# Kernel tuning notes

Measured on AMD Instinct MI355X. Metric: run time of the kernel, lower is better.

Reference implementation:

```python
import jax, jax.numpy as jnp
import numpy as np
import math

H = 16          # n_head
N_EMBD = 1024
EPS = 1e-5      # torch LayerNorm default


def setup_inputs() -> dict:
    key = jax.random.key(0)
    ks = jax.random.split(key, 6)
    B, T, C = 2, 2048, 1024
    x = jax.random.normal(ks[0], (B, T, C), dtype=jnp.float32)
    s = 0.02  # GPT-2 style init scale keeps softmax logits sane
    Wq = jax.random.normal(ks[1], (C, N_EMBD), dtype=jnp.float32) * s
    Wk = jax.random.normal(ks[2], (C, N_EMBD), dtype=jnp.float32) * s
    Wv = jax.random.normal(ks[3], (C, N_EMBD), dtype=jnp.float32) * s
    Wo = jax.random.normal(ks[4], (N_EMBD, C), dtype=jnp.float32) * s
    return {
        "x": x,
        "Wq": Wq, "bq": jnp.zeros((N_EMBD,), jnp.float32),
        "Wk": Wk, "bk": jnp.zeros((N_EMBD,), jnp.float32),
        "Wv": Wv, "bv": jnp.zeros((N_EMBD,), jnp.float32),
        "Wo": Wo, "bo": jnp.zeros((C,), jnp.float32),
        "gamma": jnp.ones((C,), jnp.float32),
        "beta": jnp.zeros((C,), jnp.float32),
    }


def reference(x, Wq, bq, Wk, bk, Wv, bv, Wo, bo, gamma, beta):
    B, T, _ = x.shape
    Dh = N_EMBD // H
    # projections -> (B, H, T, Dh)
    def split_heads(y):
        return y.reshape(B, T, H, Dh).transpose(0, 2, 1, 3)
    q = split_heads(x @ Wq + bq)
    k = split_heads(x @ Wk + bk)
    v = split_heads(x @ Wv + bv)
    # naive causal attention: explicit (B,H,T,T) scores
    att = jnp.einsum("bhtd,bhsd->bhts", q, k) * (1.0 / math.sqrt(Dh))
    causal = jnp.tril(jnp.ones((T, T), dtype=bool))
    att = jnp.where(causal[None, None], att, -jnp.inf)
    att = jax.nn.softmax(att, axis=-1)
    o = jnp.einsum("bhts,bhsd->bhtd", att, v)
    o = o.transpose(0, 2, 1, 3).reshape(B, T, N_EMBD)
    y = o @ Wo + bo
    # LayerNorm (dropout is identity at p=0 / eval)
    mu = jnp.mean(y, axis=-1, keepdims=True)
    var = jnp.var(y, axis=-1, keepdims=True)
    return (y - mu) * jax.lax.rsqrt(var + EPS) * gamma + beta
```

## Files before the change

kernel.cpp:

```cpp
#include <hip/hip_runtime.h>
#include <stdint.h>
#include <stddef.h>

typedef __attribute__((ext_vector_type(8))) short short8;
typedef __attribute__((ext_vector_type(4))) float f32x4;
typedef __attribute__((ext_vector_type(16))) float f32x16;
typedef __attribute__((ext_vector_type(4))) unsigned short us4;
typedef __attribute__((ext_vector_type(4))) unsigned u32x4;

#define DEVI static __device__ __forceinline__

DEVI unsigned short f2bf(float f) {
  unsigned u = __builtin_bit_cast(unsigned, f);
  u += 0x7FFFu + ((u >> 16) & 1u);
  return (unsigned short)(u >> 16);
}

DEVI float bf2f(unsigned short u) {
  return __builtin_bit_cast(float, ((unsigned)u) << 16);
}

DEVI f32x4 mfma16(short8 a, short8 b, f32x4 c) {
  return __builtin_amdgcn_mfma_f32_16x16x32_bf16(a, b, c, 0, 0, 0);
}

DEVI f32x16 mfma32(short8 a, short8 b, f32x16 c) {
  return __builtin_amdgcn_mfma_f32_32x32x16_bf16(a, b, c, 0, 0, 0);
}

DEVI unsigned cvtpk(float lo, float hi) {
  unsigned r;
  asm("v_cvt_pk_bf16_f32 %0, %1, %2" : "=v"(r) : "v"(lo), "v"(hi));
  return r;
}

DEVI void plswap(unsigned& a, unsigned& b) {
  asm("v_permlane32_swap_b32 %0, %1" : "+v"(a), "+v"(b));
}

DEVI float ex2(float x) {
  float r;
  asm("v_exp_f32 %0, %1" : "=v"(r) : "v"(x));
  return r;
}

DEVI float mx3(float a, float b, float c) {
  float r;
  asm("v_max3_f32 %0, %1, %2, %3" : "=v"(r) : "v"(a), "v"(b), "v"(c));
  return r;
}

DEVI f32x16 zero16() {
  f32x16 z;
#pragma unroll
  for (int i = 0; i < 16; ++i) z[i] = 0.f;
  return z;
}

DEVI void glds16(const void* g, void* l) {
  __builtin_amdgcn_global_load_lds(
      (const __attribute__((address_space(1))) void*)g,
      (__attribute__((address_space(3))) void*)l, 16, 0, 0);
}

__global__ __launch_bounds__(256) void k_cvt_x(const float* __restrict__ x,
                                               unsigned short* __restrict__ xb) {
  size_t i = ((size_t)blockIdx.x * 256 + threadIdx.x) * 8;
  f32x4 a = *(const f32x4*)(x + i);
  f32x4 b = *(const f32x4*)(x + i + 4);
  short8 v;
#pragma unroll
  for (int j = 0; j < 4; ++j) {
    v[j] = (short)f2bf(a[j]);
    v[4 + j] = (short)f2bf(b[j]);
  }
  *(short8*)(xb + i) = v;
}

__global__ __launch_bounds__(256) void k_twT4(const float* __restrict__ W0,
                                              const float* __restrict__ W1,
                                              const float* __restrict__ W2,
                                              const float* __restrict__ W3,
                                              unsigned short* __restrict__ WT) {
  __shared__ float tile[64][65];
  const int z = blockIdx.z;
  const float* W = (z == 0) ? W0 : (z == 1) ? W1 : (z == 2) ? W2 : W3;
  unsigned short* out = WT + (size_t)z * 1024 * 1024;
  const int n0 = blockIdx.x * 64, k0 = blockIdx.y * 64;
  const int t = threadIdx.x, rr = t >> 4, cc = (t & 15) * 4;
#pragma unroll
  for (int i = 0; i < 4; ++i) {
    int row = i * 16 + rr;
    f32x4 v = *(const f32x4*)(W + (size_t)(k0 + row) * 1024 + n0 + cc);
#pragma unroll
    for (int j = 0; j < 4; ++j) tile[row][cc + j] = v[j];
  }
  __syncthreads();
#pragma unroll
  for (int i = 0; i < 4; ++i) {
    int nrow = i * 16 + rr;
    us4 u;
#pragma unroll
    for (int j = 0; j < 4; ++j) u[j] = f2bf(tile[cc + j][nrow]);
    *(us4*)(out + (size_t)(n0 + nrow) * 1024 + k0 + cc) = u;
  }
}

template <bool SWAP>
DEVI void gemm_core2(const unsigned short* __restrict__ A,
                     const unsigned short* __restrict__ Bt,
                     int mt, int nt, char* lds, f32x4 (&acc)[4][4]) {
  const int t = threadIdx.x;
  const int l = t & 63, c = l & 15, g = l >> 4;
  const int w = t >> 6, wr = w >> 1, wc = w & 1;
  const int srow = t >> 3;
  const int sxor = (((t & 7) ^ (srow & 7))) * 8;
  const unsigned short* Ab = A + (size_t)(mt * 128 + srow) * 1024 + sxor;
  const unsigned short* Bb = Bt + (size_t)(nt * 128 + srow) * 1024 + sxor;
  const int key = (c & 7);

  auto STAGE = [&](int kt, int buf) {
    char* lb = lds + buf * 32768;
#pragma unroll
    for (int i = 0; i < 4; ++i) {
      glds16(Ab + (size_t)i * 32 * 1024 + kt * 64, lb + i * 4096 + t * 16);
      glds16(Bb + (size_t)i * 32 * 1024 + kt * 64, lb + 16384 + i * 4096 + t * 16);
    }
  };

  STAGE(0, 0);
  asm volatile("s_waitcnt vmcnt(0)" ::: "memory");
  __builtin_amdgcn_s_barrier();
  asm volatile("" ::: "memory");
  for (int kt = 0; kt < 16; ++kt) {
    const int cur = kt & 1;
    if (kt < 15) STAGE(kt + 1, cur ^ 1);
    const char* lb = lds + cur * 32768;
#pragma unroll
    for (int ks = 0; ks < 2; ++ks) {
      short8 af[4], bfr[4];
#pragma unroll
      for (int m = 0; m < 4; ++m)
        af[m] = *(const short8*)(lb + (wr * 64 + m * 16 + c) * 128 +
                                 ((ks * 4 + g) ^ key) * 16);
#pragma unroll
      for (int n = 0; n < 4; ++n)
        bfr[n] = *(const short8*)(lb + 16384 + (wc * 64 + n * 16 + c) * 128 +
                                  ((ks * 4 + g) ^ key) * 16);
#pragma unroll
      for (int m = 0; m < 4; ++m)
#pragma unroll
        for (int n = 0; n < 4; ++n)
          acc[m][n] = SWAP ? mfma16(bfr[n], af[m], acc[m][n])
                           : mfma16(af[m], bfr[n], acc[m][n]);
    }
    asm volatile("s_waitcnt vmcnt(0)" ::: "memory");
    __builtin_amdgcn_s_barrier();
    asm volatile("" ::: "memory");
  }
}

template <bool SWAP>
DEVI void gemm_core3(const unsigned short* __restrict__ A,
                     const unsigned short* __restrict__ Bt,
                     int mt, int nt, char* lds, f32x4 (&acc)[8][4]) {
  const int t = threadIdx.x;
  const int l = t & 63, c = l & 15, g = l >> 4;
  const int w = t >> 6, wm = w >> 2, wn = w & 3;
  const int srow = t >> 3;
  const int sxor = ((t & 7) ^ (srow & 7)) * 8;
  const unsigned short* Ab = A + (size_t)(mt * 256 + srow) * 1024 + sxor;
  const unsigned short* Bb = Bt + (size_t)(nt * 256 + srow) * 1024 + sxor;
  const int key = c & 7;

  auto STAGE = [&](int kt, int buf) {
    char* lb = lds + buf * 65536;
#pragma unroll
    for (int i = 0; i < 4; ++i) {
      glds16(Ab + (size_t)(i * 64) * 1024 + kt * 64, lb + i * 8192 + t * 16);
      glds16(Bb + (size_t)(i * 64) * 1024 + kt * 64, lb + 32768 + i * 8192 + t * 16);
    }
  };

  STAGE(0, 0);
  asm volatile("s_waitcnt vmcnt(0)" ::: "memory");
  __builtin_amdgcn_s_barrier();
  asm volatile("" ::: "memory");
  for (int kt = 0; kt < 16; ++kt) {
    const int cur = kt & 1;
    if (kt < 15) STAGE(kt + 1, cur ^ 1);
    const char* la = lds + cur * 65536;
    const char* lbB = la + 32768;
    short8 bf[4][2];
#pragma unroll
    for (int fc = 0; fc < 4; ++fc)
#pragma unroll
      for (int ks = 0; ks < 2; ++ks) {
        int brow = wn * 64 + fc * 16 + c;
        bf[fc][ks] = *(const short8*)(lbB + brow * 128 + (((ks * 4 + g) ^ key) * 16));
      }
#pragma unroll
    for (int p = 0; p < 4; ++p) {
      short8 af[2][2];
#pragma unroll
      for (int r2 = 0; r2 < 2; ++r2)
#pragma unroll
        for (int ks = 0; ks < 2; ++ks) {
          int arow = wm * 128 + (2 * p + r2) * 16 + c;
          af[r2][ks] = *(const short8*)(la + arow * 128 + (((ks * 4 + g) ^ key) * 16));
        }
      __builtin_amdgcn_s_setprio(1);
#pragma unroll
      for (int ks = 0; ks < 2; ++ks)
#pragma unroll
        for (int r2 = 0; r2 < 2; ++r2)
#pragma unroll
          for (int fc = 0; fc < 4; ++fc)
            acc[2 * p + r2][fc] = SWAP ? mfma16(bf[fc][ks], af[r2][ks], acc[2 * p + r2][fc])
                                       : mfma16(af[r2][ks], bf[fc][ks], acc[2 * p + r2][fc]);
      __builtin_amdgcn_s_setprio(0);
    }
    asm volatile("s_waitcnt vmcnt(0)" ::: "memory");
    __builtin_amdgcn_s_barrier();
    asm volatile("" ::: "memory");
  }
}

__global__ __launch_bounds__(512) void k_gemm_qkv2(
    const unsigned short* __restrict__ A,
    const unsigned short* __restrict__ Wf,
    const float* __restrict__ b0, const float* __restrict__ b1, const float* __restrict__ b2,
    unsigned short* __restrict__ O0, unsigned short* __restrict__ O1,
    unsigned short* __restrict__ O2) {
  extern __shared__ char lds[];
  const int ntz = blockIdx.x, mt = blockIdx.y;
  const int z = ntz >> 2, ntl = ntz & 3;
  const float* bias = (z == 0) ? b0 : (z == 1) ? b1 : b2;
  unsigned short* out = (z == 0) ? O0 : (z == 1) ? O1 : O2;
  f32x4 acc[8][4];
#pragma unroll
  for (int m = 0; m < 8; ++m)
#pragma unroll
    for (int n = 0; n < 4; ++n) acc[m][n] = (f32x4){0.f, 0.f, 0.f, 0.f};
  const int t = threadIdx.x, l = t & 63, c = l & 15, g = l >> 4;
  const int w = t >> 6, wm = w >> 2, wn = w & 3;
  if (z < 2) {
    gemm_core3<true>(A, Wf, mt, ntz, lds, acc);
    const float sc = (z == 0) ? 0.18033688011f : 1.0f;
#pragma unroll
    for (int fc = 0; fc < 4; ++fc) {
      int colb = ntl * 256 + wn * 64 + fc * 16 + 4 * g;
      f32x4 bv4 = *(const f32x4*)(bias + colb);
      int h = colb >> 6, d = colb & 63;
#pragma unroll
      for (int fr = 0; fr < 8; ++fr) {
        int rowg = mt * 256 + wm * 128 + fr * 16 + c;
        int b = rowg >> 11, tt = rowg & 2047;
        us4 u;
#pragma unroll
        for (int r = 0; r < 4; ++r) u[r] = f2bf((acc[fr][fc][r] + bv4[r]) * sc);
        *(us4*)(out + ((size_t)(b * 16 + h) * 2048 + tt) * 64 + d) = u;
      }
    }
  } else {
    gemm_core3<false>(A, Wf, mt, ntz, lds, acc);
#pragma unroll
    for (int fc = 0; fc < 4; ++fc) {
      int colg = ntl * 256 + wn * 64 + fc * 16 + c;
      float bvv = bias[colg];
      int h = colg >> 6, d = colg & 63;
#pragma unroll
      for (int fr = 0; fr < 8; ++fr) {
        int rowg = mt * 256 + wm * 128 + fr * 16 + 4 * g;
        int b = rowg >> 11, tt = rowg & 2047;
        us4 u;
#pragma unroll
        for (int r = 0; r < 4; ++r) u[r] = f2bf(acc[fr][fc][r] + bvv);
        *(us4*)(out + ((size_t)(b * 16 + h) * 64 + d) * 2048 + tt) = u;
      }
    }
  }
}

__global__ __launch_bounds__(256) void k_gemm_proj(const unsigned short* __restrict__ A,
                                                   const unsigned short* __restrict__ Bt,
                                                   const float* __restrict__ bias,
                                                   float* __restrict__ Y) {
  __shared__ char lds[65536];
  f32x4 acc[4][4];
#pragma unroll
  for (int m = 0; m < 4; ++m)
#pragma unroll
    for (int n = 0; n < 4; ++n) acc[m][n] = (f32x4){0.f, 0.f, 0.f, 0.f};
  const int lin = blockIdx.y * 32 + blockIdx.x;
  const int nt = lin & 7, mt = lin >> 3;
  gemm_core2<true>(A, Bt, mt, nt, lds, acc);
  const int t = threadIdx.x, l = t & 63, c = l & 15, g = l >> 4;
  const int w = t >> 6, wr = w >> 1, wc = w & 1;
#pragma unroll
  for (int n = 0; n < 4; ++n) {
    int colb = nt * 128 + wc * 64 + n * 16 + 4 * g;
    f32x4 bv4 = *(const f32x4*)(bias + colb);
#pragma unroll
    for (int m = 0; m < 4; ++m) {
      int rowg = mt * 128 + wr * 64 + m * 16 + c;
      f32x4 o;
#pragma unroll
      for (int r = 0; r < 4; ++r) o[r] = acc[m][n][r] + bv4[r];
      *(f32x4*)(Y + (size_t)rowg * 1024 + colb) = o;
    }
  }
}

__global__ __launch_bounds__(128) void k_attn5(const unsigned short* __restrict__ Q,
                                               const unsigned short* __restrict__ K,
                                               const unsigned short* __restrict__ VT,
                                               unsigned short* __restrict__ O,
                                               unsigned short* __restrict__ P,
                                               float* __restrict__ ML) {
  __shared__ char lds[32768];
  const int bid = blockIdx.x;
  int qt, c0, nt, mode, bh;
  if (bid < 512) {
    mode = 1; qt = 16 + (bid >> 5); c0 = 0; nt = 16; bh = bid & 31;
  } else {
    int rem = bid - 512;
    int v = 16 - (rem >> 6);
    int sub = rem & 63;
    bh = sub & 31;
    if (sub < 32) { mode = 0; qt = v - 1;  c0 = 0;  nt = v; }
    else          { mode = 2; qt = v + 15; c0 = 16; nt = v; }
  }
  const int t = threadIdx.x;
  const int w = t >> 6, l = t & 63;
  const int lq = l & 31, hi = l >> 5;
  const int q0 = qt * 64 + w * 32;
  const size_t kbase = (size_t)bh * 2048 * 64;
  const size_t vbase = (size_t)bh * 64 * 2048;
  const int srow = t >> 3;
  const int sx = ((t & 7) ^ (srow & 7)) * 8;

  short8 qf[4];
#pragma unroll
  for (int ds = 0; ds < 4; ++ds)
    qf[ds] = *(const short8*)(Q + kbase + (size_t)(q0 + lq) * 64 + 16 * ds + 8 * hi);

  auto STAGE = [&](int ktg, int buf) {
    const unsigned short* Kt = K + kbase + (size_t)ktg * 4096;
    const unsigned short* Vt = VT + vbase + ktg * 64;
    char* lb = lds + buf * 16384;
#pragma unroll
    for (int i = 0; i < 4; ++i) {
      int row = i * 16 + srow;
      glds16(Kt + (size_t)row * 64 + sx, lb + i * 2048 + t * 16);
      glds16(Vt + (size_t)row * 2048 + sx, lb + 8192 + i * 2048 + t * 16);
    }
  };

  f32x16 oacc[2];
  oacc[0] = zero16();
  oacc[1] = zero16();
  float m_s = -1e30f, l_s = 0.f;
  const int rx = lq & 7;

  STAGE(c0, 0);
  for (int kt = 0; kt < nt; ++kt) {
    asm volatile("s_waitcnt vmcnt(0)" ::: "memory");
    __builtin_amdgcn_s_barrier();
    asm volatile("" ::: "memory");
    if (kt + 1 < nt) STAGE(c0 + kt + 1, (kt + 1) & 1);
    const char* lb = lds + (kt & 1) * 16384;
    const int kv0 = (c0 + kt) * 64;
    short8 kf0[4], kf1[4];
#pragma unroll
    for (int ds = 0; ds < 4; ++ds) {
      int blk = ((ds * 2 + hi) ^ rx) * 16;
      kf0[ds] = *(const short8*)(lb + lq * 128 + blk);
      kf1[ds] = *(const short8*)(lb + (lq + 32) * 128 + blk);
    }
    f32x16 st0 = zero16(), st1 = zero16();
    __builtin_amdgcn_s_setprio(1);
#pragma unroll
    for (int ds = 0; ds < 4; ++ds) {
      st0 = mfma32(kf0[ds], qf[ds], st0);
      st1 = mfma32(kf1[ds], qf[ds], st1);
    }
    __builtin_amdgcn_s_setprio(0);
    short8 vf[2][4];
#pragma unroll
    for (int fd = 0; fd < 2; ++fd) {
      int d = fd * 32 + lq;
#pragma unroll
      for (int s = 0; s < 4; ++s)
        vf[fd][s] = *(const short8*)(lb + 8192 + d * 128 + (((s * 2 + hi) ^ rx) * 16));
    }
    if (mode != 1 && kt == nt - 1) {
      const int qg = q0 + lq;
#pragma unroll
      for (int r = 0; r < 16; ++r) {
        int kr = kv0 + (r & 3) + 8 * (r >> 2) + 4 * hi;
        if (kr > qg) st0[r] = -1e30f;
        if (kr + 32 > qg) st1[r] = -1e30f;
      }
    }
    float a8[8];
#pragma unroll
    for (int r = 0; r < 8; ++r)
      a8[r] = fmaxf(mx3(st0[r], st0[r + 8], st1[r]), st1[r + 8]);
    float mxv = mx3(mx3(a8[0], a8[1], a8[2]), mx3(a8[3], a8[4], a8[5]),
                    fmaxf(a8[6], a8[7]));
    if (!__all(mxv - m_s <= 11.5413f)) {
      mxv = fmaxf(mxv, __shfl_xor(mxv, 32, 64));
      float mnew = fmaxf(m_s, mxv);
      float corr = ex2(m_s - mnew);
      m_s = mnew;
      l_s *= corr;
#pragma unroll
      for (int r = 0; r < 16; ++r) {
        oacc[0][r] *= corr;
        oacc[1][r] *= corr;
      }
    }
    unsigned Wp[2][4][2];
    float gs[8];
#pragma unroll
    for (int f = 0; f < 2; ++f)
#pragma unroll
      for (int m4 = 0; m4 < 4; ++m4) {
        float p0 = ex2((f ? st1 : st0)[4 * m4 + 0] - m_s);
        float p1 = ex2((f ? st1 : st0)[4 * m4 + 1] - m_s);
        float p2 = ex2((f ? st1 : st0)[4 * m4 + 2] - m_s);
        float p3 = ex2((f ? st1 : st0)[4 * m4 + 3] - m_s);
        gs[f * 4 + m4] = (p0 + p1) + (p2 + p3);
        Wp[f][m4][0] = cvtpk(p0, p1);
        Wp[f][m4][1] = cvtpk(p2, p3);
      }
    l_s += ((gs[0] + gs[1]) + (gs[2] + gs[3])) + ((gs[4] + gs[5]) + (gs[6] + gs[7]));
    __builtin_amdgcn_s_setprio(1);
#pragma unroll
    for (int s = 0; s < 4; ++s) {
      const int f = s >> 1, s2 = s & 1;
      unsigned a0 = Wp[f][2 * s2][0], b0 = Wp[f][2 * s2 + 1][0];
      unsigned a1 = Wp[f][2 * s2][1], b1 = Wp[f][2 * s2 + 1][1];
      plswap(a0, b0);
      plswap(a1, b1);
      u32x4 pw = {a0, a1, b0, b1};
      short8 pf = __builtin_bit_cast(short8, pw);
      oacc[0] = mfma32(vf[0][s], pf, oacc[0]);
      oacc[1] = mfma32(vf[1][s], pf, oacc[1]);
    }
    __builtin_amdgcn_s_setprio(0);
  }
  l_s += __shfl_xor(l_s, 32, 64);
  if (mode == 0) {
    const float inv = 1.0f / l_s;
    const int b = bh >> 4, h = bh & 15;
    unsigned short* orow = O + ((size_t)b * 2048 + q0 + lq) * 1024 + h * 64 + 4 * hi;
#pragma unroll
    for (int f = 0; f < 2; ++f)
#pragma unroll
      for (int m4 = 0; m4 < 4; ++m4) {
        us4 u;
#pragma unroll
        for (int rr = 0; rr < 4; ++rr) u[rr] = f2bf(oacc[f][4 * m4 + rr] * inv);
        *(us4*)(orow + f * 32 + m4 * 8) = u;
      }
  } else {
    const int pid = ((qt - 16) * 32 + bh) * 2 + (mode - 1);
    unsigned short* prow = P + (size_t)pid * 4096 + (w * 32 + lq) * 64 + 4 * hi;
#pragma unroll
    for (int f = 0; f < 2; ++f)
#pragma unroll
      for (int m4 = 0; m4 < 4; ++m4) {
        us4 u;
#pragma unroll
        for (int rr = 0; rr < 4; ++rr) u[rr] = f2bf(oacc[f][4 * m4 + rr]);
        *(us4*)(prow + f * 32 + m4 * 8) = u;
      }
    if (hi == 0) {
      ML[pid * 128 + w * 32 + lq] = m_s;
      ML[pid * 128 + 64 + w * 32 + lq] = l_s;
    }
  }
}

__global__ __launch_bounds__(64) void k_merge(const unsigned short* __restrict__ P,
                                              const float* __restrict__ ML,
                                              unsigned short* __restrict__ O) {
  const int blk = blockIdx.x;
  const int qt = 16 + (blk >> 5), bh = blk & 31;
  const int pidA = ((qt - 16) * 32 + bh) * 2, pidB = pidA + 1;
  const int r = threadIdx.x;
  float mA = ML[pidA * 128 + r], lA = ML[pidA * 128 + 64 + r];
  float mB = ML[pidB * 128 + r], lB = ML[pidB * 128 + 64 + r];
  float mM = fmaxf(mA, mB);
  float wA = ex2(mA - mM), wB = ex2(mB - mM);
  float inv = 1.f / (lA * wA + lB * wB);
  wA *= inv;
  wB *= inv;
  const unsigned short* pa = P + (size_t)pidA * 4096 + r * 64;
  const unsigned short* pb = P + (size_t)pidB * 4096 + r * 64;
  const int b = bh >> 4, h = bh & 15, q = qt * 64 + r;
  unsigned short* orow = O + ((size_t)b * 2048 + q) * 1024 + h * 64;
#pragma unroll
  for (int j = 0; j < 8; ++j) {
    short8 a = *(const short8*)(pa + j * 8);
    short8 c = *(const short8*)(pb + j * 8);
    short8 o;
#pragma unroll
    for (int k = 0; k < 8; ++k)
      o[k] = (short)f2bf(bf2f((unsigned short)a[k]) * wA +
                         bf2f((unsigned short)c[k]) * wB);
    *(short8*)(orow + j * 8) = o;
  }
}

__global__ __launch_bounds__(256) void k_ln(const float* __restrict__ Y,
                                            const float* __restrict__ gamma,
                                            const float* __restrict__ beta,
                                            float* __restrict__ out) {
  __shared__ float red[8];
  const int row = blockIdx.x, t = threadIdx.x, w = t >> 6, l = t & 63;
  const float* yr = Y + (size_t)row * 1024;
  f32x4 v = *(const f32x4*)(yr + t * 4);
  float s = v[0] + v[1] + v[2] + v[3];
  float ss = v[0] * v[0] + v[1] * v[1] + v[2] * v[2] + v[3] * v[3];
#pragma unroll
  for (int d = 1; d < 64; d <<= 1) {
    s += __shfl_xor(s, d, 64);
    ss += __shfl_xor(ss, d, 64);
  }
  if (l == 0) {
    red[w] = s;
    red[4 + w] = ss;
  }
  __syncthreads();
  s = red[0] + red[1] + red[2] + red[3];
  ss = red[4] + red[5] + red[6] + red[7];
  float mean = s * (1.f / 1024.f);
  float var = ss * (1.f / 1024.f) - mean * mean;
  float rstd = rsqrtf(var + 1e-5f);
  f32x4 gv = *(const f32x4*)(gamma + t * 4);
  f32x4 bv = *(const f32x4*)(beta + t * 4);
  f32x4 ov;
#pragma unroll
  for (int j = 0; j < 4; ++j) ov[j] = (v[j] - mean) * rstd * gv[j] + bv[j];
  *(f32x4*)(out + (size_t)row * 1024 + t * 4) = ov;
}

extern "C" void kernel_launch(void* const* d_in, const int* in_sizes, int n_in,
                              void* d_out, int out_size, void* d_ws, size_t ws_size,
                              hipStream_t stream) {
  (void)in_sizes; (void)n_in; (void)out_size; (void)ws_size;
  const float* x = (const float*)d_in[0];
  const float* Wq = (const float*)d_in[1];
  const float* bq = (const float*)d_in[2];
  const float* Wk = (const float*)d_in[3];
  const float* bk = (const float*)d_in[4];
  const float* Wv = (const float*)d_in[5];
  const float* bv = (const float*)d_in[6];
  const float* Wo = (const float*)d_in[7];
  const float* bo = (const float*)d_in[8];
  const float* gamma = (const float*)d_in[9];
  const float* beta = (const float*)d_in[10];
  char* ws = (char*)d_ws;
  const size_t MB = 1024 * 1024;
  unsigned short* xb = (unsigned short*)(ws);
  unsigned short* WT = (unsigned short*)(ws + 8 * MB);
  unsigned short* WoT = (unsigned short*)(ws + 14 * MB);
  unsigned short* Qb = (unsigned short*)(ws + 16 * MB);
  unsigned short* Kb = (unsigned short*)(ws + 24 * MB);
  unsigned short* VTb = (unsigned short*)(ws + 32 * MB);
  unsigned short* Ob = (unsigned short*)(ws + 40 * MB);
  float* Y = (float*)(ws + 16 * MB);
  unsigned short* Pp = (unsigned short*)(ws);
  float* MLp = (float*)(ws + 8 * MB);

  k_cvt_x<<<2048, 256, 0, stream>>>(x, xb);
  k_twT4<<<dim3(16, 16, 4), 256, 0, stream>>>(Wq, Wk, Wv, Wo, WT);
  k_gemm_qkv2<<<dim3(12, 16), 512, 131072, stream>>>(xb, WT, bq, bk, bv, Qb, Kb, VTb);
  k_attn5<<<1536, 128, 0, stream>>>(Qb, Kb, VTb, Ob, Pp, MLp);
  k_merge<<<512, 64, 0, stream>>>(Pp, MLp, Ob);
  k_gemm_proj<<<dim3(32, 8), 256, 0, stream>>>(Ob, WoT, bo, Y);
  k_ln<<<4096, 256, 0, stream>>>(Y, gamma, beta, (float*)d_out);
}
```

Measured before the change: 115.8 us.

## Widen attention blocks to 128 query rows and store projection output as bf16

The attention kernel now uses 256-thread blocks covering 128 query rows, with four waves sharing each staged K/V tile. Per-wave tile counts let the diagonal waves stop early, and the block split, partial buffer and merge kernel are reindexed to match. This halves K/V global loads per query and halves block count, at the cost of some idle waves on causal diagonal tiles and fewer blocks for load balance. Separately, the output projection writes bf16 instead of fp32, halving that intermediate's traffic into LayerNorm at the cost of reduced precision before normalization.

```diff
diff --git a/kernel.cpp b/kernel.cpp
--- a/kernel.cpp
+++ b/kernel.cpp
@@ -285,7 +285,7 @@
 __global__ __launch_bounds__(256) void k_gemm_proj(const unsigned short* __restrict__ A,
                                                    const unsigned short* __restrict__ Bt,
                                                    const float* __restrict__ bias,
-                                                   float* __restrict__ Y) {
+                                                   unsigned short* __restrict__ Yb) {
   __shared__ char lds[65536];
   f32x4 acc[4][4];
 #pragma unroll
@@ -304,15 +304,15 @@
 #pragma unroll
     for (int m = 0; m < 4; ++m) {
       int rowg = mt * 128 + wr * 64 + m * 16 + c;
-      f32x4 o;
-#pragma unroll
-      for (int r = 0; r < 4; ++r) o[r] = acc[m][n][r] + bv4[r];
-      *(f32x4*)(Y + (size_t)rowg * 1024 + colb) = o;
-    }
-  }
-}
-
-__global__ __launch_bounds__(128) void k_attn5(const unsigned short* __restrict__ Q,
+      us4 u;
+#pragma unroll
+      for (int r = 0; r < 4; ++r) u[r] = f2bf(acc[m][n][r] + bv4[r]);
+      *(us4*)(Yb + (size_t)rowg * 1024 + colb) = u;
+    }
+  }
+}
+
+__global__ __launch_bounds__(256) void k_attn8(const unsigned short* __restrict__ Q,
                                                const unsigned short* __restrict__ K,
                                                const unsigned short* __restrict__ VT,
                                                unsigned short* __restrict__ O,
@@ -320,25 +320,26 @@
                                                float* __restrict__ ML) {
   __shared__ char lds[32768];
   const int bid = blockIdx.x;
-  int qt, c0, nt, mode, bh;
-  if (bid < 512) {
-    mode = 1; qt = 16 + (bid >> 5); c0 = 0; nt = 16; bh = bid & 31;
+  int qt, c0, NT, mode, bh;
+  if (bid < 256) {
+    mode = 1; qt = 8 + (bid >> 5); c0 = 0; NT = 16; bh = bid & 31;
   } else {
-    int rem = bid - 512;
-    int v = 16 - (rem >> 6);
+    int rem = bid - 256;
+    int lvl = rem >> 6;
     int sub = rem & 63;
     bh = sub & 31;
-    if (sub < 32) { mode = 0; qt = v - 1;  c0 = 0;  nt = v; }
-    else          { mode = 2; qt = v + 15; c0 = 16; nt = v; }
+    if (sub < 32) { mode = 0; qt = 7 - lvl;  c0 = 0;  NT = 2 * qt + 2; }
+    else          { mode = 2; qt = 15 - lvl; c0 = 16; NT = 2 * qt - 14; }
   }
   const int t = threadIdx.x;
   const int w = t >> 6, l = t & 63;
   const int lq = l & 31, hi = l >> 5;
-  const int q0 = qt * 64 + w * 32;
+  const int q0 = qt * 128 + w * 32;
   const size_t kbase = (size_t)bh * 2048 * 64;
   const size_t vbase = (size_t)bh * 64 * 2048;
   const int srow = t >> 3;
   const int sx = ((t & 7) ^ (srow & 7)) * 8;
+  const int my_nt = (mode == 1) ? 16 : (2 * qt + 1 + (w >> 1) - c0);
 
   short8 qf[4];
 #pragma unroll
@@ -350,10 +351,10 @@
     const unsigned short* Vt = VT + vbase + ktg * 64;
     char* lb = lds + buf * 16384;
 #pragma unroll
-    for (int i = 0; i < 4; ++i) {
-      int row = i * 16 + srow;
-      glds16(Kt + (size_t)row * 64 + sx, lb + i * 2048 + t * 16);
-      glds16(Vt + (size_t)row * 2048 + sx, lb + 8192 + i * 2048 + t * 16);
+    for (int i = 0; i < 2; ++i) {
+      int row = i * 32 + srow;
+      glds16(Kt + (size_t)row * 64 + sx, lb + i * 4096 + t * 16);
+      glds16(Vt + (size_t)row * 2048 + sx, lb + 8192 + i * 4096 + t * 16);
     }
   };
 
@@ -364,92 +365,94 @@
   const int rx = lq & 7;
 
   STAGE(c0, 0);
-  for (int kt = 0; kt < nt; ++kt) {
+  for (int kt = 0; kt < NT; ++kt) {
     asm volatile("s_waitcnt vmcnt(0)" ::: "memory");
     __builtin_amdgcn_s_barrier();
     asm volatile("" ::: "memory");
-    if (kt + 1 < nt) STAGE(c0 + kt + 1, (kt + 1) & 1);
-    const char* lb = lds + (kt & 1) * 16384;
-    const int kv0 = (c0 + kt) * 64;
-    short8 kf0[4], kf1[4];
-#pragma unroll
-    for (int ds = 0; ds < 4; ++ds) {
-      int blk = ((ds * 2 + hi) ^ rx) * 16;
-      kf0[ds] = *(const short8*)(lb + lq * 128 + blk);
-      kf1[ds] = *(const short8*)(lb + (lq + 32) * 128 + blk);
-    }
-    f32x16 st0 = zero16(), st1 = zero16();
-    __builtin_amdgcn_s_setprio(1);
-#pragma unroll
-    for (int ds = 0; ds < 4; ++ds) {
-      st0 = mfma32(kf0[ds], qf[ds], st0);
-      st1 = mfma32(kf1[ds], qf[ds], st1);
-    }
-    __builtin_amdgcn_s_setprio(0);
-    short8 vf[2][4];
-#pragma unroll
-    for (int fd = 0; fd < 2; ++fd) {
-      int d = fd * 32 + lq;
-#pragma unroll
-      for (int s = 0; s < 4; ++s)
-        vf[fd][s] = *(const short8*)(lb + 8192 + d * 128 + (((s * 2 + hi) ^ rx) * 16));
-    }
-    if (mode != 1 && kt == nt - 1) {
-      const int qg = q0 + lq;
-#pragma unroll
-      for (int r = 0; r < 16; ++r) {
-        int kr = kv0 + (r & 3) + 8 * (r >> 2) + 4 * hi;
-        if (kr > qg) st0[r] = -1e30f;
-        if (kr + 32 > qg) st1[r] = -1e30f;
-      }
-    }
-    float a8[8];
-#pragma unroll
-    for (int r = 0; r < 8; ++r)
-      a8[r] = fmaxf(mx3(st0[r], st0[r + 8], st1[r]), st1[r + 8]);
-    float mxv = mx3(mx3(a8[0], a8[1], a8[2]), mx3(a8[3], a8[4], a8[5]),
-                    fmaxf(a8[6], a8[7]));
-    if (!__all(mxv - m_s <= 11.5413f)) {
-      mxv = fmaxf(mxv, __shfl_xor(mxv, 32, 64));
-      float mnew = fmaxf(m_s, mxv);
-      float corr = ex2(m_s - mnew);
-      m_s = mnew;
-      l_s *= corr;
-#pragma unroll
-      for (int r = 0; r < 16; ++r) {
-        oacc[0][r] *= corr;
-        oacc[1][r] *= corr;
-      }
-    }
-    unsigned Wp[2][4][2];
-    float gs[8];
-#pragma unroll
-    for (int f = 0; f < 2; ++f)
-#pragma unroll
-      for (int m4 = 0; m4 < 4; ++m4) {
-        float p0 = ex2((f ? st1 : st0)[4 * m4 + 0] - m_s);
-        float p1 = ex2((f ? st1 : st0)[4 * m4 + 1] - m_s);
-        float p2 = ex2((f ? st1 : st0)[4 * m4 + 2] - m_s);
-        float p3 = ex2((f ? st1 : st0)[4 * m4 + 3] - m_s);
-        gs[f * 4 + m4] = (p0 + p1) + (p2 + p3);
-        Wp[f][m4][0] = cvtpk(p0, p1);
-        Wp[f][m4][1] = cvtpk(p2, p3);
-      }
-    l_s += ((gs[0] + gs[1]) + (gs[2] + gs[3])) + ((gs[4] + gs[5]) + (gs[6] + gs[7]));
-    __builtin_amdgcn_s_setprio(1);
-#pragma unroll
-    for (int s = 0; s < 4; ++s) {
-      const int f = s >> 1, s2 = s & 1;
-      unsigned a0 = Wp[f][2 * s2][0], b0 = Wp[f][2 * s2 + 1][0];
-      unsigned a1 = Wp[f][2 * s2][1], b1 = Wp[f][2 * s2 + 1][1];
-      plswap(a0, b0);
-      plswap(a1, b1);
-      u32x4 pw = {a0, a1, b0, b1};
-      short8 pf = __builtin_bit_cast(short8, pw);
-      oacc[0] = mfma32(vf[0][s], pf, oacc[0]);
-      oacc[1] = mfma32(vf[1][s], pf, oacc[1]);
-    }
-    __builtin_amdgcn_s_setprio(0);
+    if (kt + 1 < NT) STAGE(c0 + kt + 1, (kt + 1) & 1);
+    if (kt < my_nt) {
+      const char* lb = lds + (kt & 1) * 16384;
+      const int kv0 = (c0 + kt) * 64;
+      short8 kf0[4], kf1[4];
+#pragma unroll
+      for (int ds = 0; ds < 4; ++ds) {
+        int blk = ((ds * 2 + hi) ^ rx) * 16;
+        kf0[ds] = *(const short8*)(lb + lq * 128 + blk);
+        kf1[ds] = *(const short8*)(lb + (lq + 32) * 128 + blk);
+      }
+      f32x16 st0 = zero16(), st1 = zero16();
+      __builtin_amdgcn_s_setprio(1);
+#pragma unroll
+      for (int ds = 0; ds < 4; ++ds) {
+        st0 = mfma32(kf0[ds], qf[ds], st0);
+        st1 = mfma32(kf1[ds], qf[ds], st1);
+      }
+      __builtin_amdgcn_s_setprio(0);
+      short8 vf[2][4];
+#pragma unroll
+      for (int fd = 0; fd < 2; ++fd) {
+        int d = fd * 32 + lq;
+#pragma unroll
+        for (int s = 0; s < 4; ++s)
+          vf[fd][s] = *(const short8*)(lb + 8192 + d * 128 + (((s * 2 + hi) ^ rx) * 16));
+      }
+      if (mode != 1 && kt == my_nt - 1) {
+        const int qg = q0 + lq;
+#pragma unroll
+        for (int r = 0; r < 16; ++r) {
+          int kr = kv0 + (r & 3) + 8 * (r >> 2) + 4 * hi;
+          if (kr > qg) st0[r] = -1e30f;
+          if (kr + 32 > qg) st1[r] = -1e30f;
+        }
+      }
+      float a8[8];
+#pragma unroll
+      for (int r = 0; r < 8; ++r)
+        a8[r] = fmaxf(mx3(st0[r], st0[r + 8], st1[r]), st1[r + 8]);
+      float mxv = mx3(mx3(a8[0], a8[1], a8[2]), mx3(a8[3], a8[4], a8[5]),
+                      fmaxf(a8[6], a8[7]));
+      if (!__all(mxv - m_s <= 11.5413f)) {
+        mxv = fmaxf(mxv, __shfl_xor(mxv, 32, 64));
+        float mnew = fmaxf(m_s, mxv);
+        float corr = ex2(m_s - mnew);
+        m_s = mnew;
+        l_s *= corr;
+#pragma unroll
+        for (int r = 0; r < 16; ++r) {
+          oacc[0][r] *= corr;
+          oacc[1][r] *= corr;
+        }
+      }
+      unsigned Wp[2][4][2];
+      float gs[8];
+#pragma unroll
+      for (int f = 0; f < 2; ++f)
+#pragma unroll
+        for (int m4 = 0; m4 < 4; ++m4) {
+          float p0 = ex2((f ? st1 : st0)[4 * m4 + 0] - m_s);
+          float p1 = ex2((f ? st1 : st0)[4 * m4 + 1] - m_s);
+          float p2 = ex2((f ? st1 : st0)[4 * m4 + 2] - m_s);
+          float p3 = ex2((f ? st1 : st0)[4 * m4 + 3] - m_s);
+          gs[f * 4 + m4] = (p0 + p1) + (p2 + p3);
+          Wp[f][m4][0] = cvtpk(p0, p1);
+          Wp[f][m4][1] = cvtpk(p2, p3);
+        }
+      l_s += ((gs[0] + gs[1]) + (gs[2] + gs[3])) + ((gs[4] + gs[5]) + (gs[6] + gs[7]));
+      __builtin_amdgcn_s_setprio(1);
+#pragma unroll
+      for (int s = 0; s < 4; ++s) {
+        const int f = s >> 1, s2 = s & 1;
+        unsigned a0 = Wp[f][2 * s2][0], b0 = Wp[f][2 * s2 + 1][0];
+        unsigned a1 = Wp[f][2 * s2][1], b1 = Wp[f][2 * s2 + 1][1];
+        plswap(a0, b0);
+        plswap(a1, b1);
+        u32x4 pw = {a0, a1, b0, b1};
+        short8 pf = __builtin_bit_cast(short8, pw);
+        oacc[0] = mfma32(vf[0][s], pf, oacc[0]);
+        oacc[1] = mfma32(vf[1][s], pf, oacc[1]);
+      }
+      __builtin_amdgcn_s_setprio(0);
+    }
   }
   l_s += __shfl_xor(l_s, 32, 64);
   if (mode == 0) {
@@ -466,8 +469,9 @@
         *(us4*)(orow + f * 32 + m4 * 8) = u;
       }
   } else {
-    const int pid = ((qt - 16) * 32 + bh) * 2 + (mode - 1);
-    unsigned short* prow = P + (size_t)pid * 4096 + (w * 32 + lq) * 64 + 4 * hi;
+    const int pid = ((qt - 8) * 32 + bh) * 2 + (mode - 1);
+    const int row = w * 32 + lq;
+    unsigned short* prow = P + (size_t)pid * 8192 + row * 64 + 4 * hi;
 #pragma unroll
     for (int f = 0; f < 2; ++f)
 #pragma unroll
@@ -478,29 +482,29 @@
         *(us4*)(prow + f * 32 + m4 * 8) = u;
       }
     if (hi == 0) {
-      ML[pid * 128 + w * 32 + lq] = m_s;
-      ML[pid * 128 + 64 + w * 32 + lq] = l_s;
-    }
-  }
-}
-
-__global__ __launch_bounds__(64) void k_merge(const unsigned short* __restrict__ P,
-                                              const float* __restrict__ ML,
-                                              unsigned short* __restrict__ O) {
+      ML[pid * 256 + row] = m_s;
+      ML[pid * 256 + 128 + row] = l_s;
+    }
+  }
+}
+
+__global__ __launch_bounds__(128) void k_merge(const unsigned short* __restrict__ P,
+                                               const float* __restrict__ ML,
+                                               unsigned short* __restrict__ O) {
   const int blk = blockIdx.x;
-  const int qt = 16 + (blk >> 5), bh = blk & 31;
-  const int pidA = ((qt - 16) * 32 + bh) * 2, pidB = pidA + 1;
+  const int qt = 8 + (blk >> 5), bh = blk & 31;
+  const int pidA = ((qt - 8) * 32 + bh) * 2, pidB = pidA + 1;
   const int r = threadIdx.x;
-  float mA = ML[pidA * 128 + r], lA = ML[pidA * 128 + 64 + r];
-  float mB = ML[pidB * 128 + r], lB = ML[pidB * 128 + 64 + r];
+  float mA = ML[pidA * 256 + r], lA = ML[pidA * 256 + 128 + r];
+  float mB = ML[pidB * 256 + r], lB = ML[pidB * 256 + 128 + r];
   float mM = fmaxf(mA, mB);
   float wA = ex2(mA - mM), wB = ex2(mB - mM);
   float inv = 1.f / (lA * wA + lB * wB);
   wA *= inv;
   wB *= inv;
-  const unsigned short* pa = P + (size_t)pidA * 4096 + r * 64;
-  const unsigned short* pb = P + (size_t)pidB * 4096 + r * 64;
-  const int b = bh >> 4, h = bh & 15, q = qt * 64 + r;
+  const unsigned short* pa = P + (size_t)pidA * 8192 + r * 64;
+  const unsigned short* pb = P + (size_t)pidB * 8192 + r * 64;
+  const int b = bh >> 4, h = bh & 15, q = qt * 128 + r;
   unsigned short* orow = O + ((size_t)b * 2048 + q) * 1024 + h * 64;
 #pragma unroll
   for (int j = 0; j < 8; ++j) {
@@ -515,14 +519,16 @@
   }
 }
 
-__global__ __launch_bounds__(256) void k_ln(const float* __restrict__ Y,
+__global__ __launch_bounds__(256) void k_ln(const unsigned short* __restrict__ Yb,
                                             const float* __restrict__ gamma,
                                             const float* __restrict__ beta,
                                             float* __restrict__ out) {
   __shared__ float red[8];
   const int row = blockIdx.x, t = threadIdx.x, w = t >> 6, l = t & 63;
-  const float* yr = Y + (size_t)row * 1024;
-  f32x4 v = *(const f32x4*)(yr + t * 4);
+  us4 vb = *(const us4*)(Yb + (size_t)row * 1024 + t * 4);
+  f32x4 v;
+#pragma unroll
+  for (int j = 0; j < 4; ++j) v[j] = bf2f(vb[j]);
   float s = v[0] + v[1] + v[2] + v[3];
   float ss = v[0] * v[0] + v[1] * v[1] + v[2] * v[2] + v[3] * v[3];
 #pragma unroll
@@ -572,15 +578,15 @@
   unsigned short* Kb = (unsigned short*)(ws + 24 * MB);
   unsigned short* VTb = (unsigned short*)(ws + 32 * MB);
   unsigned short* Ob = (unsigned short*)(ws + 40 * MB);
-  float* Y = (float*)(ws + 16 * MB);
+  unsigned short* Yb = (unsigned short*)(ws + 16 * MB);
   unsigned short* Pp = (unsigned short*)(ws);
   float* MLp = (float*)(ws + 8 * MB);
 
   k_cvt_x<<<2048, 256, 0, stream>>>(x, xb);
   k_twT4<<<dim3(16, 16, 4), 256, 0, stream>>>(Wq, Wk, Wv, Wo, WT);
   k_gemm_qkv2<<<dim3(12, 16), 512, 131072, stream>>>(xb, WT, bq, bk, bv, Qb, Kb, VTb);
-  k_attn5<<<1536, 128, 0, stream>>>(Qb, Kb, VTb, Ob, Pp, MLp);
-  k_merge<<<512, 64, 0, stream>>>(Pp, MLp, Ob);
-  k_gemm_proj<<<dim3(32, 8), 256, 0, stream>>>(Ob, WoT, bo, Y);
-  k_ln<<<4096, 256, 0, stream>>>(Y, gamma, beta, (float*)d_out);
-}
+  k_attn8<<<768, 256, 0, stream>>>(Qb, Kb, VTb, Ob, Pp, MLp);
+  k_merge<<<256, 128, 0, stream>>>(Pp, MLp, Ob);
+  k_gemm_proj<<<dim3(32, 8), 256, 0, stream>>>(Ob, WoT, bo, Yb);
+  k_ln<<<4096, 256, 0, stream>>>(Yb, gamma, beta, (float*)d_out);
+}
```

Measured after the change: 115.1 us. No clear change (-0.6%).
